# Kernel optimization log

Measured on AMD Instinct MI355X. Metric: run time of the kernel, lower is better.

Reference implementation:

```python
import jax, jax.numpy as jnp
import numpy as np

B, L, E, H = 2, 4096, 1024, 16
D = E // H          # head_dim = 64
CHUNK = 256         # matches the torch module's chunk_size


def setup_inputs() -> dict:
    key = jax.random.key(0)
    k1, k2, k3 = jax.random.split(key, 3)
    x = jax.random.normal(k1, (B, L, E), dtype=jnp.float32)
    # torch Linear weight layout: (out_features, in_features); y = x @ W.T
    W_qkv = jax.random.normal(k2, (3 * E, E), dtype=jnp.float32) * 0.02
    W_out = jax.random.normal(k3, (E, E), dtype=jnp.float32) * 0.02
    return {"x": x, "W_qkv": W_qkv, "W_out": W_out}


def _linear_attention(x, W_qkv, W_out):
    Bz, Lz, Ez = x.shape
    scale = D ** (-0.5)
    qkv = x @ W_qkv.T                                # [B, L, 3E]
    qkv = qkv.reshape(Bz, Lz, 3, H, D).transpose(2, 0, 3, 1, 4)  # [3, B, H, L, D]
    q, k, v = qkv[0], qkv[1], qkv[2]
    # feature map: elu(x) + 1, query also scaled by head_dim^-0.5
    q = (jax.nn.elu(q) + 1.0) * scale
    k = jax.nn.elu(k) + 1.0

    nc = Lz // CHUNK  # seq_len chosen divisible by CHUNK
    def to_chunks(t):  # [B,H,L,D] -> [nc, B, H, CHUNK, D]
        return t.reshape(Bz, H, nc, CHUNK, D).transpose(2, 0, 1, 3, 4)
    qc, kc, vc = to_chunks(q), to_chunks(k), to_chunks(v)

    causal = jnp.tril(jnp.ones((CHUNK, CHUNK), dtype=x.dtype))

    def step(carry, inp):
        S, Z = carry                     # S: [B,H,D,D], Z: [B,H,D]
        qi, ki, vi = inp                 # each [B,H,CHUNK,D]
        # intra-chunk causal contribution (same math as cumsum of k v^T outer products)
        attn = jnp.einsum('bhld,bhmd->bhlm', qi, ki) * causal
        num = jnp.einsum('bhlm,bhme->bhle', attn, vi) + jnp.einsum('bhld,bhde->bhle', qi, S)
        den = attn.sum(-1) + jnp.einsum('bhld,bhd->bhl', qi, Z)
        S = S + jnp.einsum('bhmd,bhme->bhde', ki, vi)
        Z = Z + ki.sum(axis=2)
        return (S, Z), (num, den)

    S0 = jnp.zeros((Bz, H, D, D), dtype=x.dtype)
    Z0 = jnp.zeros((Bz, H, D), dtype=x.dtype)
    _, (num, den) = jax.lax.scan(step, (S0, Z0), (qc, kc, vc))
    # [nc,B,H,CHUNK,D] -> [B,H,L,D]
    num = num.transpose(1, 2, 0, 3, 4).reshape(Bz, H, Lz, D)
    den = den.transpose(1, 2, 0, 3).reshape(Bz, H, Lz)
    den = jnp.maximum(den, 1e-6)
    out = num / den[..., None]
    out = out.transpose(0, 2, 1, 3).reshape(Bz, Lz, Ez)
    return out @ W_out.T


def reference(x, W_qkv, W_out):
    return _linear_attention(x, W_qkv, W_out)
```

## Files before the change

### kernel.cpp

```cpp
#include <hip/hip_runtime.h>
#include <hip/hip_bf16.h>
#include <math.h>

#define B_ 2
#define L_ 4096
#define E_ 1024
#define H_ 16
#define D_ 64
#define CK_ 64
#define NC_ 64

typedef __bf16 bf16x8 __attribute__((ext_vector_type(8)));
typedef __bf16 bf16x4 __attribute__((ext_vector_type(4)));
typedef float  f32x4  __attribute__((ext_vector_type(4)));

__device__ __forceinline__ float fmap1(float x) { return x > 0.f ? x + 1.f : expf(x); }
__device__ __forceinline__ float b2f(__bf16 v) {
    __hip_bfloat16 h = *reinterpret_cast<__hip_bfloat16*>(&v); return __bfloat162float(h);
}
__device__ __forceinline__ __bf16 f2b(float f) {
    __hip_bfloat16 h = __float2bfloat16(f); return *reinterpret_cast<__bf16*>(&h);
}
__device__ __forceinline__ unsigned short f2u(float f) {
    __hip_bfloat16 h = __float2bfloat16(f); return *reinterpret_cast<unsigned short*>(&h);
}

union U8 { bf16x8 v; __bf16 e[8]; bf16x4 half2[2]; };

__device__ __forceinline__ void async16(const __bf16* g, __bf16* lds) {
    __builtin_amdgcn_global_load_lds(
        (const __attribute__((address_space(1))) void*)g,
        (__attribute__((address_space(3))) void*)lds, 16, 0, 0);
}

__global__ __launch_bounds__(256) void cast_f32_bf16(const float* __restrict__ in,
                                                     __hip_bfloat16* __restrict__ out, int n) {
    int i = (blockIdx.x * 256 + threadIdx.x) << 2;
    if (i < n) {
        float4 v = *(const float4*)(in + i);
        ushort4 o = {f2u(v.x), f2u(v.y), f2u(v.z), f2u(v.w)};
        *(ushort4*)(out + i) = o;
    }
}

template<int EPI>
__global__ __launch_bounds__(256) void gemm_mfma(const __bf16* __restrict__ A,
                                                 const __bf16* __restrict__ Bw,
                                                 void* __restrict__ Cv,
                                                 __hip_bfloat16* __restrict__ KT,
                                                 __hip_bfloat16* __restrict__ VT,
                                                 int M, int N, int K) {
    __shared__ alignas(16) __bf16 As[128 * 32];
    __shared__ alignas(16) __bf16 Bs[128 * 32];
    const int tid = threadIdx.x;
    const int wave = tid >> 6, lane = tid & 63;
    const int wm = wave >> 1, wn = wave & 1;
    const int lq = lane >> 4, lr = lane & 15;
    const int m0 = blockIdx.y * 128, n0 = blockIdx.x * 128;

    f32x4 acc[4][4];
#pragma unroll
    for (int i = 0; i < 4; ++i)
#pragma unroll
        for (int j = 0; j < 4; ++j) acc[i][j] = (f32x4){0.f, 0.f, 0.f, 0.f};

    const int stg_r = lane >> 2, stg_c = (lane & 3) << 3;
    const __bf16* Ag0 = A + (size_t)(m0 + (wave << 4) + stg_r) * K + stg_c;
    const __bf16* Ag1 = A + (size_t)(m0 + 64 + (wave << 4) + stg_r) * K + stg_c;
    const __bf16* Bg0 = Bw + (size_t)(n0 + (wave << 4) + stg_r) * K + stg_c;
    const __bf16* Bg1 = Bw + (size_t)(n0 + 64 + (wave << 4) + stg_r) * K + stg_c;
    __bf16* Al0 = As + (wave << 9);
    __bf16* Al1 = As + ((wave + 4) << 9);
    __bf16* Bl0 = Bs + (wave << 9);
    __bf16* Bl1 = Bs + ((wave + 4) << 9);

    for (int kt = 0; kt < K; kt += 32) {
        __syncthreads();
        async16(Ag0 + kt, Al0);
        async16(Ag1 + kt, Al1);
        async16(Bg0 + kt, Bl0);
        async16(Bg1 + kt, Bl1);
        __syncthreads();
        bf16x8 af[4], bfr[4];
#pragma unroll
        for (int t = 0; t < 4; ++t) {
            af[t]  = *(const bf16x8*)&As[((wm << 6) + (t << 4) + lr) * 32 + (lq << 3)];
            bfr[t] = *(const bf16x8*)&Bs[((wn << 6) + (t << 4) + lr) * 32 + (lq << 3)];
        }
#pragma unroll
        for (int mt = 0; mt < 4; ++mt)
#pragma unroll
            for (int nt = 0; nt < 4; ++nt)
                acc[mt][nt] = __builtin_amdgcn_mfma_f32_16x16x32_bf16(
                    af[mt], bfr[nt], acc[mt][nt], 0, 0, 0);
    }

#pragma unroll
    for (int mt = 0; mt < 4; ++mt) {
#pragma unroll
        for (int nt = 0; nt < 4; ++nt) {
            int m = m0 + (wm << 6) + (mt << 4) + (lq << 2);
            int n = n0 + (wn << 6) + (nt << 4) + lr;
            if (EPI == 1) {
                int w = n >> 10, hh = (n >> 6) & 15, dd = n & 63;
                float vv[4];
#pragma unroll
                for (int r = 0; r < 4; ++r) {
                    float v = acc[mt][nt][r];
                    if (w == 0)      v = fmap1(v) * 0.125f;
                    else if (w == 1) v = fmap1(v);
                    vv[r] = v;
                    ((__hip_bfloat16*)Cv)[(size_t)(m + r) * N + n] = __float2bfloat16(v);
                }
                if (w >= 1) {
                    int b = m >> 12, l = m & 4095;
                    __hip_bfloat16* T = (w == 1) ? KT : VT;
                    ushort4 u = {f2u(vv[0]), f2u(vv[1]), f2u(vv[2]), f2u(vv[3])};
                    *(ushort4*)&T[((size_t)((b * 16 + hh) * 64 + dd) << 12) + l] = u;
                }
            } else {
#pragma unroll
                for (int r = 0; r < 4; ++r)
                    ((float*)Cv)[(size_t)(m + r) * N + n] = acc[mt][nt][r];
            }
        }
    }
}

__global__ __launch_bounds__(256) void chunk_state_mfma(const __hip_bfloat16* __restrict__ KTh,
                                                        const __hip_bfloat16* __restrict__ VTh,
                                                        __hip_bfloat16* __restrict__ Sb,
                                                        __hip_bfloat16* __restrict__ Zb) {
    const int tid = threadIdx.x, wave = tid >> 6, lane = tid & 63;
    const int quad = lane >> 4, lr = lane & 15;
    const int bh = blockIdx.y;
    const int c = blockIdx.x * 4 + wave;
    const __bf16* KT = (const __bf16*)KTh;
    const __bf16* VT = (const __bf16*)VTh;

    bf16x8 vt[4][2], kt[4][2];
#pragma unroll
    for (int t = 0; t < 4; ++t)
#pragma unroll
        for (int kk = 0; kk < 2; ++kk) {
            size_t rowoff = ((size_t)(bh * 64 + t * 16 + lr) << 12) + c * CK_ + kk * 32 + quad * 8;
            vt[t][kk] = *(const bf16x8*)&VT[rowoff];
            kt[t][kk] = *(const bf16x8*)&KT[rowoff];
        }

    U8 of;
#pragma unroll
    for (int j = 0; j < 8; ++j) of.e[j] = f2b(1.0f);

    __hip_bfloat16* Sp = Sb + ((size_t)(c * 32 + bh) << 12);
#pragma unroll
    for (int es = 0; es < 4; ++es) {
#pragma unroll
        for (int dt = 0; dt < 4; ++dt) {
            f32x4 acc = (f32x4){0.f, 0.f, 0.f, 0.f};
            acc = __builtin_amdgcn_mfma_f32_16x16x32_bf16(vt[es][0], kt[dt][0], acc, 0, 0, 0);
            acc = __builtin_amdgcn_mfma_f32_16x16x32_bf16(vt[es][1], kt[dt][1], acc, 0, 0, 0);
#pragma unroll
            for (int r = 0; r < 4; ++r)
                Sp[(es * 16 + quad * 4 + r) * 64 + dt * 16 + lr] =
                    __float2bfloat16(acc[r]);
        }
    }
#pragma unroll
    for (int dt = 0; dt < 4; ++dt) {
        f32x4 z = (f32x4){0.f, 0.f, 0.f, 0.f};
        z = __builtin_amdgcn_mfma_f32_16x16x32_bf16(kt[dt][0], of.v, z, 0, 0, 0);
        z = __builtin_amdgcn_mfma_f32_16x16x32_bf16(kt[dt][1], of.v, z, 0, 0, 0);
        if (lr == 0) {
#pragma unroll
            for (int r = 0; r < 4; ++r)
                Zb[((c * 32 + bh) << 6) + dt * 16 + quad * 4 + r] = __float2bfloat16(z[r]);
        }
    }
}

__global__ __launch_bounds__(256) void prefix64(__hip_bfloat16* __restrict__ Sb,
                                                __hip_bfloat16* __restrict__ Zb) {
    const int bh = blockIdx.y;
    const int idx = blockIdx.x * 256 + threadIdx.x;
    float run = 0.f;
    for (int c = 0; c < NC_; ++c) {
        size_t off = ((size_t)(c * 32 + bh) << 12) + idx;
        float cur = __bfloat162float(Sb[off]);
        Sb[off] = __float2bfloat16(run);
        run += cur;
    }
    if (blockIdx.x == 0 && threadIdx.x < 64) {
        float zr = 0.f;
        for (int c = 0; c < NC_; ++c) {
            int zoff = ((c * 32 + bh) << 6) + threadIdx.x;
            float cz = __bfloat162float(Zb[zoff]);
            Zb[zoff] = __float2bfloat16(zr);
            zr += cz;
        }
    }
}

__global__ __launch_bounds__(256) void attn_out_mfma(const __hip_bfloat16* __restrict__ qvh,
                                                     const __hip_bfloat16* __restrict__ Sbh,
                                                     const __hip_bfloat16* __restrict__ Zbh,
                                                     const __hip_bfloat16* __restrict__ VTh,
                                                     __hip_bfloat16* __restrict__ attn) {
    __shared__ __bf16 Pbuf[4 * 64 * 68];
    const int tid = threadIdx.x, wave = tid >> 6, lane = tid & 63;
    const int quad = lane >> 4, lr = lane & 15;
    const int bh = blockIdx.y, b = bh >> 4, h = bh & 15;
    const int c = blockIdx.x * 4 + wave;
    const size_t t0 = (size_t)b * L_ + c * CK_;
    const __bf16* qb = (const __bf16*)qvh;
    const __bf16* Sb = (const __bf16*)Sbh;
    const __bf16* Zb = (const __bf16*)Zbh;
    const __bf16* VT = (const __bf16*)VTh;
    __bf16* P = Pbuf + wave * (64 * 68);

    bf16x8 qf[4][2];
#pragma unroll
    for (int ls = 0; ls < 4; ++ls)
#pragma unroll
        for (int kk = 0; kk < 2; ++kk)
            qf[ls][kk] = *(const bf16x8*)&qb[(t0 + ls * 16 + lr) * 3072 + h * 64 + kk * 32 + quad * 8];

    f32x4 num[4][4], den[4];
#pragma unroll
    for (int i = 0; i < 4; ++i) {
        den[i] = (f32x4){0.f, 0.f, 0.f, 0.f};
#pragma unroll
        for (int j = 0; j < 4; ++j) num[i][j] = (f32x4){0.f, 0.f, 0.f, 0.f};
    }

    bf16x8 zf[2];
#pragma unroll
    for (int kk = 0; kk < 2; ++kk)
        zf[kk] = *(const bf16x8*)&Zb[((size_t)(c * 32 + bh) << 6) + kk * 32 + quad * 8];
#pragma unroll
    for (int ls = 0; ls < 4; ++ls)
#pragma unroll
        for (int kk = 0; kk < 2; ++kk)
            den[ls] = __builtin_amdgcn_mfma_f32_16x16x32_bf16(qf[ls][kk], zf[kk], den[ls], 0, 0, 0);

#pragma unroll
    for (int es = 0; es < 4; ++es) {
        bf16x8 sf[2];
#pragma unroll
        for (int kk = 0; kk < 2; ++kk)
            sf[kk] = *(const bf16x8*)&Sb[((size_t)(c * 32 + bh) << 12)
                                         + (es * 16 + lr) * 64 + kk * 32 + quad * 8];
#pragma unroll
        for (int ls = 0; ls < 4; ++ls)
#pragma unroll
            for (int kk = 0; kk < 2; ++kk)
                num[ls][es] = __builtin_amdgcn_mfma_f32_16x16x32_bf16(
                    qf[ls][kk], sf[kk], num[ls][es], 0, 0, 0);
    }

    bf16x8 kf[4][2];
#pragma unroll
    for (int ms = 0; ms < 4; ++ms)
#pragma unroll
        for (int kk = 0; kk < 2; ++kk)
            kf[ms][kk] = *(const bf16x8*)&qb[(t0 + ms * 16 + lr) * 3072 + 1024 + h * 64 + kk * 32 + quad * 8];

#pragma unroll
    for (int ls = 0; ls < 4; ++ls) {
#pragma unroll
        for (int ms = 0; ms < 4; ++ms) {
            int off = (ls * 16 + lr) * 68 + ms * 16 + quad * 4;
            if (ms <= ls) {
                f32x4 pt = (f32x4){0.f, 0.f, 0.f, 0.f};
                pt = __builtin_amdgcn_mfma_f32_16x16x32_bf16(kf[ms][0], qf[ls][0], pt, 0, 0, 0);
                pt = __builtin_amdgcn_mfma_f32_16x16x32_bf16(kf[ms][1], qf[ls][1], pt, 0, 0, 0);
                ushort4 u;
                if (ms == ls) {
                    u.x = (quad * 4 + 0 > lr) ? 0 : f2u(pt[0]);
                    u.y = (quad * 4 + 1 > lr) ? 0 : f2u(pt[1]);
                    u.z = (quad * 4 + 2 > lr) ? 0 : f2u(pt[2]);
                    u.w = (quad * 4 + 3 > lr) ? 0 : f2u(pt[3]);
                } else {
                    u = (ushort4){f2u(pt[0]), f2u(pt[1]), f2u(pt[2]), f2u(pt[3])};
                }
                *(ushort4*)&P[off] = u;
            } else {
                *(ushort4*)&P[off] = (ushort4){0, 0, 0, 0};
            }
        }
    }

    U8 of;
#pragma unroll
    for (int j = 0; j < 8; ++j) of.e[j] = f2b(1.0f);

#pragma unroll
    for (int kk = 0; kk < 2; ++kk) {
        U8 pf[4];
#pragma unroll
        for (int ls = 0; ls < 4; ++ls) {
            pf[ls].half2[0] = *(const bf16x4*)&P[(ls * 16 + lr) * 68 + kk * 32 + quad * 8];
            pf[ls].half2[1] = *(const bf16x4*)&P[(ls * 16 + lr) * 68 + kk * 32 + quad * 8 + 4];
        }
        bf16x8 vf[4];
#pragma unroll
        for (int es = 0; es < 4; ++es)
            vf[es] = *(const bf16x8*)&VT[((size_t)((b * 16 + h) * 64 + es * 16 + lr) << 12)
                                         + c * CK_ + kk * 32 + quad * 8];
#pragma unroll
        for (int ls = 0; ls < 4; ++ls) {
            den[ls] = __builtin_amdgcn_mfma_f32_16x16x32_bf16(pf[ls].v, of.v, den[ls], 0, 0, 0);
#pragma unroll
            for (int es = 0; es < 4; ++es)
                num[ls][es] = __builtin_amdgcn_mfma_f32_16x16x32_bf16(
                    pf[ls].v, vf[es], num[ls][es], 0, 0, 0);
        }
    }

#pragma unroll
    for (int ls = 0; ls < 4; ++ls) {
#pragma unroll
        for (int r = 0; r < 4; ++r) {
            float inv = 1.f / fmaxf(den[ls][r], 1e-6f);
            size_t row = (t0 + ls * 16 + quad * 4 + r) * 1024 + h * 64;
#pragma unroll
            for (int es = 0; es < 4; ++es)
                attn[row + es * 16 + lr] = __float2bfloat16(num[ls][es][r] * inv);
        }
    }
}

extern "C" void kernel_launch(void* const* d_in, const int* in_sizes, int n_in,
                              void* d_out, int out_size, void* d_ws, size_t ws_size,
                              hipStream_t stream) {
    (void)ws_size; (void)out_size;
    const float *x = nullptr, *Wqkv = nullptr, *Wout = nullptr;
    for (int i = 0; i < n_in; ++i) {
        if (in_sizes[i] == 8388608)      x    = (const float*)d_in[i];
        else if (in_sizes[i] == 3145728) Wqkv = (const float*)d_in[i];
        else if (in_sizes[i] == 1048576) Wout = (const float*)d_in[i];
    }

    __hip_bfloat16* ws16  = (__hip_bfloat16*)d_ws;
    __hip_bfloat16* xb    = ws16;
    __hip_bfloat16* attn  = ws16;
    __hip_bfloat16* Wqkvb = ws16 + 8388608;
    __hip_bfloat16* Woutb = Wqkvb + 3145728;
    __hip_bfloat16* qv    = Woutb + 1048576;
    __hip_bfloat16* VT    = qv + 25165824;
    __hip_bfloat16* KT    = VT + 8388608;
    __hip_bfloat16* Sb    = KT + 8388608;
    __hip_bfloat16* Zb    = Sb + 8388608;

    cast_f32_bf16<<<8388608 / 1024, 256, 0, stream>>>(x, xb, 8388608);
    cast_f32_bf16<<<3145728 / 1024, 256, 0, stream>>>(Wqkv, Wqkvb, 3145728);
    cast_f32_bf16<<<1048576 / 1024, 256, 0, stream>>>(Wout, Woutb, 1048576);

    gemm_mfma<1><<<dim3(3072 / 128, 8192 / 128), 256, 0, stream>>>(
        (const __bf16*)xb, (const __bf16*)Wqkvb, qv, KT, VT, B_ * L_, 3 * E_, E_);
    chunk_state_mfma<<<dim3(16, B_ * H_), 256, 0, stream>>>(KT, VT, Sb, Zb);
    prefix64<<<dim3(16, B_ * H_), 256, 0, stream>>>(Sb, Zb);
    attn_out_mfma<<<dim3(16, B_ * H_), 256, 0, stream>>>(qv, Sb, Zb, VT, attn);
    gemm_mfma<0><<<dim3(1024 / 128, 8192 / 128), 256, 0, stream>>>(
        (const __bf16*)attn, (const __bf16*)Woutb, d_out, nullptr, nullptr, B_ * L_, E_, E_);
}
```

Measured before the change: 247.6 us.

## Replace QKV projection GEMM with 256x256-tile pipelined MFMA kernel

Adds a new 512-thread GEMM for the QKV projection that uses 256x256 output tiles and BK=64. It double-buffers LDS with async global-to-LDS loads staged in quarters, interleaved with the MFMA sub-blocks, and uses s_setprio and explicit waitcnt barriers. The fused epilogue (feature map, scaling, K/V transposed writes) is kept. The aim is more data reuse per loaded byte and overlap of memory with compute. The trade-off is heavy register pressure and a grid of only 384 blocks, which may leave the GPU's CUs underfilled.

```diff
diff --git a/kernel.cpp b/kernel.cpp
--- a/kernel.cpp
+++ b/kernel.cpp
@@ -41,6 +41,153 @@
         ushort4 o = {f2u(v.x), f2u(v.y), f2u(v.z), f2u(v.w)};
         *(ushort4*)(out + i) = o;
     }
+}
+
+__global__ __launch_bounds__(512, 2) void gemm256_qkv(const __bf16* __restrict__ A,
+                                                      const __bf16* __restrict__ Bw,
+                                                      __hip_bfloat16* __restrict__ C,
+                                                      __hip_bfloat16* __restrict__ KT,
+                                                      __hip_bfloat16* __restrict__ VT,
+                                                      int M, int N, int K) {
+    __shared__ alignas(16) __bf16 ldsA[2][16384];
+    __shared__ alignas(16) __bf16 ldsB[2][16384];
+    const int tid  = threadIdx.x;
+    const int wave = tid >> 6, lane = tid & 63;
+    const int wm = wave >> 2, wn = wave & 3;
+    const int lq = lane >> 4, lr = lane & 15;
+    const int m0 = blockIdx.y << 8, n0 = blockIdx.x << 8;
+    const int NT = K >> 6;
+
+    f32x4 acc[8][4];
+#pragma unroll
+    for (int i = 0; i < 8; ++i)
+#pragma unroll
+        for (int j = 0; j < 4; ++j) acc[i][j] = (f32x4){0.f, 0.f, 0.f, 0.f};
+
+    const int srow = lane >> 2;
+    const int scol = ((lane & 3) << 3) ^ ((lane >> 5) << 4);
+    const __bf16* Ab0 = A  + (size_t)(m0 + wm * 128 + wn * 16 + srow) * K + scol;
+    const __bf16* Ab1 = Ab0 + (size_t)64 * K;
+    const __bf16* Bb0 = Bw + (size_t)(n0 + wn * 64 + wm * 16 + srow) * K + scol;
+    const __bf16* Bb1 = Bb0 + (size_t)32 * K;
+    const int saoff0 = (wm * 8 + wn) << 10;
+    const int saoff1 = (wm * 8 + 4 + wn) << 10;
+    const int sboff0 = (wn * 4 + wm) << 10;
+    const int sboff1 = (wn * 4 + 2 + wm) << 10;
+
+#define STG_A0(bufi, kt) do { const __bf16* g_ = Ab0 + ((size_t)(kt) << 6); \
+    async16(g_,      &ldsA[bufi][saoff0]); \
+    async16(g_ + 32, &ldsA[bufi][saoff0 + 512]); } while (0)
+#define STG_A1(bufi, kt) do { const __bf16* g_ = Ab1 + ((size_t)(kt) << 6); \
+    async16(g_,      &ldsA[bufi][saoff1]); \
+    async16(g_ + 32, &ldsA[bufi][saoff1 + 512]); } while (0)
+#define STG_B0(bufi, kt) do { const __bf16* g_ = Bb0 + ((size_t)(kt) << 6); \
+    async16(g_,      &ldsB[bufi][sboff0]); \
+    async16(g_ + 32, &ldsB[bufi][sboff0 + 512]); } while (0)
+#define STG_B1(bufi, kt) do { const __bf16* g_ = Bb1 + ((size_t)(kt) << 6); \
+    async16(g_,      &ldsB[bufi][sboff1]); \
+    async16(g_ + 32, &ldsB[bufi][sboff1 + 512]); } while (0)
+
+    const int inn = (lr << 6) + ((lq << 4) ^ ((lr & 8) << 2));
+    bf16x8 af[4][2], bfr[2][2][2];
+
+#define LDA(qm) { const char* p_ = (const char*)ldsA[cur]; \
+    _Pragma("unroll") for (int mt = 0; mt < 4; ++mt) \
+    _Pragma("unroll") for (int ks = 0; ks < 2; ++ks) \
+        af[mt][ks] = *(const bf16x8*)(p_ + ((((wm * 8 + (qm) * 4 + mt) << 1) + ks) << 10) + inn); }
+#define LDB(qn) { const char* p_ = (const char*)ldsB[cur]; \
+    _Pragma("unroll") for (int nt = 0; nt < 2; ++nt) \
+    _Pragma("unroll") for (int ks = 0; ks < 2; ++ks) \
+        bfr[qn][nt][ks] = *(const bf16x8*)(p_ + ((((wn * 4 + (qn) * 2 + nt) << 1) + ks) << 10) + inn); }
+#define MM(qm, qn) { \
+    _Pragma("unroll") for (int mt = 0; mt < 4; ++mt) \
+    _Pragma("unroll") for (int nt = 0; nt < 2; ++nt) { \
+        acc[(qm)*4+mt][(qn)*2+nt] = __builtin_amdgcn_mfma_f32_16x16x32_bf16( \
+            af[mt][0], bfr[qn][nt][0], acc[(qm)*4+mt][(qn)*2+nt], 0, 0, 0); \
+        acc[(qm)*4+mt][(qn)*2+nt] = __builtin_amdgcn_mfma_f32_16x16x32_bf16( \
+            af[mt][1], bfr[qn][nt][1], acc[(qm)*4+mt][(qn)*2+nt], 0, 0, 0); } }
+#define BAR() __builtin_amdgcn_s_barrier()
+#define WLG0() do { asm volatile("s_waitcnt lgkmcnt(0)" ::: "memory"); \
+    __builtin_amdgcn_sched_barrier(0); } while (0)
+#define WVM(n) do { asm volatile("s_waitcnt vmcnt(" #n ")" ::: "memory"); \
+    __builtin_amdgcn_sched_barrier(0); } while (0)
+
+    STG_B0(0, 0); STG_B1(0, 0); STG_A0(0, 0); STG_A1(0, 0);
+    STG_B0(1, 1); STG_B1(1, 1); STG_A0(1, 1);
+    WVM(6);
+    BAR();
+
+    for (int t = 0; t < NT; ++t) {
+        const int cur = t & 1;
+        LDA(0); LDB(0);
+        if (t + 1 < NT) STG_A1(cur ^ 1, t + 1);
+        BAR();
+        WLG0();
+        __builtin_amdgcn_s_setprio(1);
+        MM(0, 0);
+        __builtin_amdgcn_s_setprio(0);
+        BAR();
+        LDB(1);
+        if (t + 2 < NT) STG_B0(cur, t + 2);
+        BAR();
+        WLG0();
+        __builtin_amdgcn_s_setprio(1);
+        MM(0, 1);
+        __builtin_amdgcn_s_setprio(0);
+        BAR();
+        LDA(1);
+        if (t + 2 < NT) STG_B1(cur, t + 2);
+        BAR();
+        WLG0();
+        __builtin_amdgcn_s_setprio(1);
+        MM(1, 0);
+        __builtin_amdgcn_s_setprio(0);
+        BAR();
+        if (t + 2 < NT) STG_A0(cur, t + 2);
+        BAR();
+        __builtin_amdgcn_s_setprio(1);
+        MM(1, 1);
+        __builtin_amdgcn_s_setprio(0);
+        if (t < NT - 2)       { WVM(6); }
+        else if (t == NT - 2) { WVM(0); }
+        BAR();
+    }
+
+    const int w = n0 >> 10;
+#pragma unroll
+    for (int i = 0; i < 8; ++i) {
+        const int m = m0 + wm * 128 + i * 16 + lq * 4;
+        const int bb = m >> 12, l = m & 4095;
+#pragma unroll
+        for (int j = 0; j < 4; ++j) {
+            const int n = n0 + wn * 64 + j * 16 + lr;
+            float vv[4];
+#pragma unroll
+            for (int r = 0; r < 4; ++r) {
+                float v = acc[i][j][r];
+                if (w == 0)      v = fmap1(v) * 0.125f;
+                else if (w == 1) v = fmap1(v);
+                vv[r] = v;
+                C[(size_t)(m + r) * N + n] = __float2bfloat16(v);
+            }
+            if (w >= 1) {
+                const int hh = (n >> 6) & 15, dd = n & 63;
+                __hip_bfloat16* T = (w == 1) ? KT : VT;
+                ushort4 u = {f2u(vv[0]), f2u(vv[1]), f2u(vv[2]), f2u(vv[3])};
+                *(ushort4*)&T[((size_t)((bb * 16 + hh) * 64 + dd) << 12) + l] = u;
+            }
+        }
+    }
+#undef STG_A0
+#undef STG_A1
+#undef STG_B0
+#undef STG_B1
+#undef LDA
+#undef LDB
+#undef MM
+#undef BAR
+#undef WLG0
+#undef WVM
 }
 
 template<int EPI>
@@ -356,7 +503,7 @@
     cast_f32_bf16<<<3145728 / 1024, 256, 0, stream>>>(Wqkv, Wqkvb, 3145728);
     cast_f32_bf16<<<1048576 / 1024, 256, 0, stream>>>(Wout, Woutb, 1048576);
 
-    gemm_mfma<1><<<dim3(3072 / 128, 8192 / 128), 256, 0, stream>>>(
+    gemm256_qkv<<<dim3(3072 / 256, 8192 / 256), 512, 0, stream>>>(
         (const __bf16*)xb, (const __bf16*)Wqkvb, qv, KT, VT, B_ * L_, 3 * E_, E_);
     chunk_state_mfma<<<dim3(16, B_ * H_), 256, 0, stream>>>(KT, VT, Sb, Zb);
     prefix64<<<dim3(16, B_ * H_), 256, 0, stream>>>(Sb, Zb);
```

After: 250.3 us. About the same (+1.1%).

## Triple-buffer GEMM LDS tiles with async global-to-LDS prefetch two stages ahead

Applied to the files above, without the earlier changes.

Replaces the single-buffered GEMM main loop, which had two barriers per K-step and exposed load latency, with a three-stage LDS ring. Tiles for step t+2 are issued asynchronously while MFMAs run on step t, and explicit vmcnt waits plus one barrier per iteration keep ordering. This aims to hide global memory latency in both projection GEMMs, at the cost of three times the LDS per block, which may reduce occupancy.

```diff
diff --git a/kernel.cpp b/kernel.cpp
--- a/kernel.cpp
+++ b/kernel.cpp
@@ -43,20 +43,24 @@
     }
 }
 
+#define WVMC(n) do { asm volatile("s_waitcnt vmcnt(" #n ")" ::: "memory"); \
+    __builtin_amdgcn_sched_barrier(0); } while (0)
+
 template<int EPI>
-__global__ __launch_bounds__(256) void gemm_mfma(const __bf16* __restrict__ A,
-                                                 const __bf16* __restrict__ Bw,
-                                                 void* __restrict__ Cv,
-                                                 __hip_bfloat16* __restrict__ KT,
-                                                 __hip_bfloat16* __restrict__ VT,
-                                                 int M, int N, int K) {
-    __shared__ alignas(16) __bf16 As[128 * 32];
-    __shared__ alignas(16) __bf16 Bs[128 * 32];
+__global__ __launch_bounds__(256) void gemm_mfma3(const __bf16* __restrict__ A,
+                                                  const __bf16* __restrict__ Bw,
+                                                  void* __restrict__ Cv,
+                                                  __hip_bfloat16* __restrict__ KT,
+                                                  __hip_bfloat16* __restrict__ VT,
+                                                  int M, int N, int K) {
+    __shared__ alignas(16) __bf16 As[3][128 * 32];
+    __shared__ alignas(16) __bf16 Bs[3][128 * 32];
     const int tid = threadIdx.x;
     const int wave = tid >> 6, lane = tid & 63;
     const int wm = wave >> 1, wn = wave & 1;
     const int lq = lane >> 4, lr = lane & 15;
     const int m0 = blockIdx.y * 128, n0 = blockIdx.x * 128;
+    const int NS = K >> 5;
 
     f32x4 acc[4][4];
 #pragma unroll
@@ -69,23 +73,27 @@
     const __bf16* Ag1 = A + (size_t)(m0 + 64 + (wave << 4) + stg_r) * K + stg_c;
     const __bf16* Bg0 = Bw + (size_t)(n0 + (wave << 4) + stg_r) * K + stg_c;
     const __bf16* Bg1 = Bw + (size_t)(n0 + 64 + (wave << 4) + stg_r) * K + stg_c;
-    __bf16* Al0 = As + (wave << 9);
-    __bf16* Al1 = As + ((wave + 4) << 9);
-    __bf16* Bl0 = Bs + (wave << 9);
-    __bf16* Bl1 = Bs + ((wave + 4) << 9);
-
-    for (int kt = 0; kt < K; kt += 32) {
-        __syncthreads();
-        async16(Ag0 + kt, Al0);
-        async16(Ag1 + kt, Al1);
-        async16(Bg0 + kt, Bl0);
-        async16(Bg1 + kt, Bl1);
-        __syncthreads();
+    const int dl0 = (wave << 9), dl1 = ((wave + 4) << 9);
+
+#define STG3(bi, t) do { const int ko_ = (t) << 5; \
+    async16(Ag0 + ko_, &As[bi][dl0]); \
+    async16(Ag1 + ko_, &As[bi][dl1]); \
+    async16(Bg0 + ko_, &Bs[bi][dl0]); \
+    async16(Bg1 + ko_, &Bs[bi][dl1]); } while (0)
+
+    STG3(0, 0);
+    STG3(1, 1);
+    WVMC(4);
+    __builtin_amdgcn_s_barrier();
+
+    int bi = 0, bn = 2;
+    for (int t = 0; t < NS; ++t) {
+        if (t + 2 < NS) STG3(bn, t + 2);
         bf16x8 af[4], bfr[4];
 #pragma unroll
-        for (int t = 0; t < 4; ++t) {
-            af[t]  = *(const bf16x8*)&As[((wm << 6) + (t << 4) + lr) * 32 + (lq << 3)];
-            bfr[t] = *(const bf16x8*)&Bs[((wn << 6) + (t << 4) + lr) * 32 + (lq << 3)];
+        for (int tt = 0; tt < 4; ++tt) {
+            af[tt]  = *(const bf16x8*)&As[bi][((wm << 6) + (tt << 4) + lr) * 32 + (lq << 3)];
+            bfr[tt] = *(const bf16x8*)&Bs[bi][((wn << 6) + (tt << 4) + lr) * 32 + (lq << 3)];
         }
 #pragma unroll
         for (int mt = 0; mt < 4; ++mt)
@@ -93,6 +101,11 @@
             for (int nt = 0; nt < 4; ++nt)
                 acc[mt][nt] = __builtin_amdgcn_mfma_f32_16x16x32_bf16(
                     af[mt], bfr[nt], acc[mt][nt], 0, 0, 0);
+        if (t < NS - 2)       { WVMC(4); }
+        else if (t == NS - 2) { WVMC(0); }
+        __builtin_amdgcn_s_barrier();
+        bi = (bi == 2) ? 0 : bi + 1;
+        bn = (bn == 2) ? 0 : bn + 1;
     }
 
 #pragma unroll
@@ -125,6 +138,7 @@
             }
         }
     }
+#undef STG3
 }
 
 __global__ __launch_bounds__(256) void chunk_state_mfma(const __hip_bfloat16* __restrict__ KTh,
@@ -356,11 +370,11 @@
     cast_f32_bf16<<<3145728 / 1024, 256, 0, stream>>>(Wqkv, Wqkvb, 3145728);
     cast_f32_bf16<<<1048576 / 1024, 256, 0, stream>>>(Wout, Woutb, 1048576);
 
-    gemm_mfma<1><<<dim3(3072 / 128, 8192 / 128), 256, 0, stream>>>(
+    gemm_mfma3<1><<<dim3(3072 / 128, 8192 / 128), 256, 0, stream>>>(
         (const __bf16*)xb, (const __bf16*)Wqkvb, qv, KT, VT, B_ * L_, 3 * E_, E_);
     chunk_state_mfma<<<dim3(16, B_ * H_), 256, 0, stream>>>(KT, VT, Sb, Zb);
     prefix64<<<dim3(16, B_ * H_), 256, 0, stream>>>(Sb, Zb);
     attn_out_mfma<<<dim3(16, B_ * H_), 256, 0, stream>>>(qv, Sb, Zb, VT, attn);
-    gemm_mfma<0><<<dim3(1024 / 128, 8192 / 128), 256, 0, stream>>>(
+    gemm_mfma3<0><<<dim3(1024 / 128, 8192 / 128), 256, 0, stream>>>(
         (const __bf16*)attn, (const __bf16*)Woutb, d_out, nullptr, nullptr, B_ * L_, E_, E_);
 }
```

New measurement: 244.4 us. About the same (-1.3%).
